# Optimization experiments

Hardware: AMD Instinct MI355X
Metric: run time of the kernel (lower is better)

Reference implementation:

```python
import jax, jax.numpy as jnp
import numpy as np

B, N, M = 2, 8192, 8192


def setup_inputs() -> dict:
    key = jax.random.key(0)
    ks = jax.random.split(key, 6)
    return {
        "predicted_points": jax.random.normal(ks[0], (B, N, 3), dtype=jnp.float32),
        "predicted_sdfs": jax.random.normal(ks[1], (B, N, 1), dtype=jnp.float32),
        "predicted_colors": jax.random.uniform(ks[2], (B, N, 3), dtype=jnp.float32),
        "ref_points": jax.random.normal(ks[3], (B, M, 3), dtype=jnp.float32),
        "ref_sdfs": jax.random.normal(ks[4], (B, M, 1), dtype=jnp.float32),
        "ref_colors": jax.random.uniform(ks[5], (B, M, 3), dtype=jnp.float32),
    }


def reference(predicted_points, predicted_sdfs, predicted_colors,
              ref_points, ref_sdfs, ref_colors):
    # Squared pairwise distances [B, N, M]; monotonic in cdist, so argmin/min
    # match torch.cdist-based results (chamfer_distance uses squared dists).
    d2 = (jnp.sum(predicted_points ** 2, axis=-1)[:, :, None]
          + jnp.sum(ref_points ** 2, axis=-1)[:, None, :]
          - 2.0 * jnp.einsum("bnd,bmd->bnm", predicted_points, ref_points))
    d2 = jnp.maximum(d2, 0.0)

    # Faithful to original: argmin over dim=1 -> nearest PREDICTED point index
    # for each ref point, shape [B, M]; then gathers into ref_sdfs/ref_colors.
    closest = jnp.argmin(d2, axis=1)  # [B, M], values in [0, N)

    gathered_sdfs = jnp.take_along_axis(ref_sdfs, closest[..., None], axis=1)  # [B, M, 1]
    sdf_l1 = jnp.mean(jnp.abs(gathered_sdfs - predicted_sdfs))

    gathered_colors = jnp.take_along_axis(ref_colors, closest[..., None], axis=1)  # [B, M, 3]
    color_l1 = jnp.mean(jnp.abs(gathered_colors - predicted_colors))

    # pytorch3d chamfer_distance: mean over points of squared min dists in both
    # directions, summed, then mean over batch.
    cham_xy = jnp.mean(jnp.min(d2, axis=2), axis=1)  # pred -> ref, [B]
    cham_yx = jnp.mean(jnp.min(d2, axis=1), axis=1)  # ref -> pred, [B]
    chamfer = jnp.mean(cham_xy + cham_yx)

    # [sdf_l1_loss, color_l1_loss, chamfer_distance_loss]
    return jnp.stack([sdf_l1, color_l1, chamfer])
```

## Files before the change

kernel.cpp:

```cpp
#include <hip/hip_runtime.h>
#include <cstdint>
#include <cstddef>

#define B_ 2
#define N_ 8192
#define M_ 8192
#define COLSPLIT 8
#define CCHUNK (N_ / COLSPLIT)
#define NTILES (CCHUNK / 32)
#define ROWS_PER_WAVE 32
#define ROWS_PER_BLOCK 128
#define RBLOCKS ((B_ * M_) / 256)

typedef __attribute__((ext_vector_type(8))) short short8;
typedef __attribute__((ext_vector_type(16))) float f32x16;

union FragU { uint4 u; short8 s; };

__device__ __forceinline__ unsigned bf16r(float f) {
    unsigned u = __float_as_uint(f);
    return ((u + 0x7FFFu + ((u >> 16) & 1u)) >> 16) & 0xFFFFu;
}
#define BF_ONE 0x3F80u

__device__ __forceinline__ unsigned umin_(unsigned a, unsigned b) { return a < b ? a : b; }

__global__ __launch_bounds__(256) void k_init(uint4* __restrict__ p)
{
    const int i = blockIdx.x * 256 + threadIdx.x;
    uint4 v = {0xFFFFFFFFu, 0xFFFFFFFFu, 0xFFFFFFFFu, 0xFFFFFFFFu};
    p[i] = v;
}

__global__ __launch_bounds__(256, 4) void k_pairs(
    const float* __restrict__ pred_pts,
    const float* __restrict__ ref_pts,
    unsigned long long* __restrict__ packed,
    unsigned int* __restrict__ colminU)
{
    __shared__ uint4 ldsB[CCHUNK + 1];
    __shared__ unsigned int ldsCol[CCHUNK];

    const int t    = threadIdx.x;
    const int wave = t >> 6;
    const int lane = t & 63;
    const int l31  = lane & 31;
    const int half = lane >> 5;
    const int rowblk  = blockIdx.x;
    const int colbase = blockIdx.y * CCHUNK;
    const int b       = blockIdx.z;

    for (int i = t; i < CCHUNK; i += 256) {
        const float* p = pred_pts + ((size_t)b * N_ + colbase + i) * 3;
        float x = p[0], y = p[1], z = p[2];
        float nrm = x * x + y * y + z * z;
        unsigned nh = bf16r(nrm);
        unsigned nl = bf16r(nrm - __uint_as_float(nh << 16));
        uint4 v;
        v.x = bf16r(-2.f * x) | (bf16r(-2.f * y) << 16);
        v.y = bf16r(-2.f * z) | (BF_ONE << 16);
        v.z = BF_ONE | (nh << 16);
        v.w = nl;
        ldsB[i] = v;
        ldsCol[i] = 0xFFFFFFFFu;
    }
    if (t == 0) { uint4 z4 = {0, 0, 0, 0}; ldsB[CCHUNK] = z4; }

    FragU af; af.u.x = af.u.y = af.u.z = af.u.w = 0;
    const int rowbase = rowblk * ROWS_PER_BLOCK + wave * ROWS_PER_WAVE;
    if (half == 0) {
        const float* r = ref_pts + ((size_t)b * M_ + rowbase + l31) * 3;
        float x = r[0], y = r[1], z = r[2];
        float nrm = x * x + y * y + z * z;
        unsigned nh = bf16r(nrm);
        unsigned nl = bf16r(nrm - __uint_as_float(nh << 16));
        af.u.x = bf16r(x) | (bf16r(y) << 16);
        af.u.y = bf16r(z) | (nh << 16);
        af.u.z = nl | (BF_ONE << 16);
        af.u.w = BF_ONE;
    }
    __syncthreads();

    f32x16 zero16 = {};
    unsigned rowbest[16];
    #pragma unroll
    for (int i = 0; i < 16; ++i) rowbest[i] = 0xFFFFFFFFu;

    const int bslot = (half == 0) ? l31 : CCHUNK;
    const int bstep = (half == 0) ? 32 : 0;

    #pragma unroll 2
    for (int tile = 0; tile < NTILES; tile += 2) {
        FragU b0; b0.u = ldsB[bslot + tile * bstep];
        FragU b1; b1.u = ldsB[bslot + (tile + 1) * bstep];
        f32x16 acc0 = __builtin_amdgcn_mfma_f32_32x32x16_bf16(af.s, b0.s, zero16, 0, 0, 0);
        f32x16 acc1 = __builtin_amdgcn_mfma_f32_32x32x16_bf16(af.s, b1.s, zero16, 0, 0, 0);

        const unsigned lcol0 = (unsigned)(tile * 32 + l31);
        const unsigned lcol1 = lcol0 + 32;
        #pragma unroll
        for (int i = 0; i < 16; ++i) {
            unsigned pk0 = (__float_as_uint(acc0[i]) & 0xFFFFF800u) | lcol0;
            unsigned pk1 = (__float_as_uint(acc1[i]) & 0xFFFFF800u) | lcol1;
            rowbest[i] = umin_(rowbest[i], umin_(pk0, pk1));
        }
        float c0 = fminf(fminf(fminf(fminf(acc0[0], acc0[1]), fminf(acc0[2], acc0[3])),
                               fminf(fminf(acc0[4], acc0[5]), fminf(acc0[6], acc0[7]))),
                         fminf(fminf(fminf(acc0[8], acc0[9]), fminf(acc0[10], acc0[11])),
                               fminf(fminf(acc0[12], acc0[13]), fminf(acc0[14], acc0[15]))));
        float c1 = fminf(fminf(fminf(fminf(acc1[0], acc1[1]), fminf(acc1[2], acc1[3])),
                               fminf(fminf(acc1[4], acc1[5]), fminf(acc1[6], acc1[7]))),
                         fminf(fminf(fminf(acc1[8], acc1[9]), fminf(acc1[10], acc1[11])),
                               fminf(fminf(acc1[12], acc1[13]), fminf(acc1[14], acc1[15]))));
        atomicMin(&ldsCol[lcol0], __float_as_uint(c0));
        atomicMin(&ldsCol[lcol1], __float_as_uint(c1));
    }

    #pragma unroll
    for (int i = 0; i < 16; ++i) {
        unsigned pk = rowbest[i];
        #pragma unroll
        for (int off = 1; off < 32; off <<= 1) {
            unsigned o = __shfl_xor(pk, off);
            pk = o < pk ? o : pk;
        }
        if (l31 == 0) {
            int row = rowbase + (i & 3) + 8 * (i >> 2) + 4 * half;
            unsigned long long v =
                ((unsigned long long)(pk & 0xFFFFF800u) << 32)
                | (unsigned)(colbase + (pk & 0x7FFu));
            atomicMin(&packed[(size_t)b * M_ + row], v);
        }
    }

    __syncthreads();
    for (int i = t; i < CCHUNK; i += 256)
        atomicMin(&colminU[(size_t)b * N_ + colbase + i], ldsCol[i]);
}

__global__ __launch_bounds__(256) void k_reduce(
    const unsigned long long* __restrict__ packed,
    const unsigned int* __restrict__ colminU,
    const float* __restrict__ pred_sdfs,
    const float* __restrict__ pred_cols,
    const float* __restrict__ ref_sdfs,
    const float* __restrict__ ref_cols,
    float* __restrict__ partials)
{
    __shared__ float wsum[4][3];
    const int i = blockIdx.x * 256 + threadIdx.x;
    const int b = i >> 13;

    unsigned long long pk = packed[i];
    float chyx = fmaxf(__uint_as_float((unsigned)(pk >> 32)), 0.f);
    int arg = (int)(unsigned)(pk & 0xFFFFFFFFull);
    float chxy = fmaxf(__uint_as_float(colminU[i]), 0.f);

    float sdf = fabsf(ref_sdfs[(size_t)b * M_ + arg] - pred_sdfs[i]);
    const float* rc = ref_cols + ((size_t)b * M_ + arg) * 3;
    const float* pc = pred_cols + (size_t)i * 3;
    float col = fabsf(rc[0] - pc[0]) + fabsf(rc[1] - pc[1]) + fabsf(rc[2] - pc[2]);

    float cham = chyx * (1.f / (B_ * M_)) + chxy * (1.f / (B_ * N_));
    sdf *= 1.f / (B_ * M_);
    col *= 1.f / (B_ * M_ * 3);

    #pragma unroll
    for (int off = 32; off > 0; off >>= 1) {
        sdf  += __shfl_down(sdf, off);
        col  += __shfl_down(col, off);
        cham += __shfl_down(cham, off);
    }
    const int wave = threadIdx.x >> 6;
    if ((threadIdx.x & 63) == 0) {
        wsum[wave][0] = sdf; wsum[wave][1] = col; wsum[wave][2] = cham;
    }
    __syncthreads();
    if (threadIdx.x == 0) {
        partials[0 * RBLOCKS + blockIdx.x] = wsum[0][0] + wsum[1][0] + wsum[2][0] + wsum[3][0];
        partials[1 * RBLOCKS + blockIdx.x] = wsum[0][1] + wsum[1][1] + wsum[2][1] + wsum[3][1];
        partials[2 * RBLOCKS + blockIdx.x] = wsum[0][2] + wsum[1][2] + wsum[2][2] + wsum[3][2];
    }
}

__global__ void k_final(const float* __restrict__ partials, float* __restrict__ out)
{
    const int t = threadIdx.x;
    float s0 = partials[0 * RBLOCKS + t];
    float s1 = partials[1 * RBLOCKS + t];
    float s2 = partials[2 * RBLOCKS + t];
    #pragma unroll
    for (int off = 32; off > 0; off >>= 1) {
        s0 += __shfl_down(s0, off);
        s1 += __shfl_down(s1, off);
        s2 += __shfl_down(s2, off);
    }
    if (t == 0) { out[0] = s0; out[1] = s1; out[2] = s2; }
}

extern "C" void kernel_launch(void* const* d_in, const int* in_sizes, int n_in,
                              void* d_out, int out_size, void* d_ws, size_t ws_size,
                              hipStream_t stream) {
    const float* pred_pts  = (const float*)d_in[0];
    const float* pred_sdfs = (const float*)d_in[1];
    const float* pred_cols = (const float*)d_in[2];
    const float* ref_pts   = (const float*)d_in[3];
    const float* ref_sdfs  = (const float*)d_in[4];
    const float* ref_cols  = (const float*)d_in[5];
    float* out = (float*)d_out;

    char* ws = (char*)d_ws;
    unsigned long long* packed = (unsigned long long*)ws;
    unsigned int* colminU = (unsigned int*)(ws + (size_t)B_ * M_ * 8);
    float* partials = (float*)(ws + (size_t)B_ * M_ * 8 + (size_t)B_ * N_ * 4);

    k_init<<<48, 256, 0, stream>>>((uint4*)ws);

    dim3 g1(M_ / ROWS_PER_BLOCK, COLSPLIT, B_);
    k_pairs<<<g1, 256, 0, stream>>>(pred_pts, ref_pts, packed, colminU);

    k_reduce<<<RBLOCKS, 256, 0, stream>>>(
        packed, colminU, pred_sdfs, pred_cols, ref_sdfs, ref_cols, partials);

    k_final<<<1, 64, 0, stream>>>(partials, out);
}
```

Before: 90.12 us.

## Replace global atomics with per-split partial buffers and drop init/final kernels

```diff
diff --git a/kernel.cpp b/kernel.cpp
--- a/kernel.cpp
+++ b/kernel.cpp
@@ -8,8 +8,7 @@
 #define COLSPLIT 8
 #define CCHUNK (N_ / COLSPLIT)
 #define NTILES (CCHUNK / 32)
-#define ROWS_PER_WAVE 32
-#define ROWS_PER_BLOCK 128
+#define ROWBLKS (M_ / 128)
 #define RBLOCKS ((B_ * M_) / 256)
 
 typedef __attribute__((ext_vector_type(8))) short short8;
@@ -24,19 +23,14 @@
 #define BF_ONE 0x3F80u
 
 __device__ __forceinline__ unsigned umin_(unsigned a, unsigned b) { return a < b ? a : b; }
-
-__global__ __launch_bounds__(256) void k_init(uint4* __restrict__ p)
-{
-    const int i = blockIdx.x * 256 + threadIdx.x;
-    uint4 v = {0xFFFFFFFFu, 0xFFFFFFFFu, 0xFFFFFFFFu, 0xFFFFFFFFu};
-    p[i] = v;
-}
+__device__ __forceinline__ unsigned long long ullmin_(unsigned long long a, unsigned long long b) { return a < b ? a : b; }
 
 __global__ __launch_bounds__(256, 4) void k_pairs(
     const float* __restrict__ pred_pts,
     const float* __restrict__ ref_pts,
-    unsigned long long* __restrict__ packed,
-    unsigned int* __restrict__ colminU)
+    unsigned long long* __restrict__ rowpart,
+    unsigned int* __restrict__ colpart,
+    float* __restrict__ out)
 {
     __shared__ uint4 ldsB[CCHUNK + 1];
     __shared__ unsigned int ldsCol[CCHUNK];
@@ -47,8 +41,13 @@
     const int l31  = lane & 31;
     const int half = lane >> 5;
     const int rowblk  = blockIdx.x;
-    const int colbase = blockIdx.y * CCHUNK;
+    const int cs      = blockIdx.y;
+    const int colbase = cs * CCHUNK;
     const int b       = blockIdx.z;
+
+    if (rowblk == 0 && cs == 0 && b == 0 && t == 0) {
+        out[0] = 0.f; out[1] = 0.f; out[2] = 0.f;
+    }
 
     for (int i = t; i < CCHUNK; i += 256) {
         const float* p = pred_pts + ((size_t)b * N_ + colbase + i) * 3;
@@ -67,7 +66,7 @@
     if (t == 0) { uint4 z4 = {0, 0, 0, 0}; ldsB[CCHUNK] = z4; }
 
     FragU af; af.u.x = af.u.y = af.u.z = af.u.w = 0;
-    const int rowbase = rowblk * ROWS_PER_BLOCK + wave * ROWS_PER_WAVE;
+    const int rowbase = rowblk * 128 + wave * 32;
     if (half == 0) {
         const float* r = ref_pts + ((size_t)b * M_ + rowbase + l31) * 3;
         float x = r[0], y = r[1], z = r[2];
@@ -116,6 +115,7 @@
         atomicMin(&ldsCol[lcol1], __float_as_uint(c1));
     }
 
+    unsigned long long* rdst = rowpart + (size_t)(b * COLSPLIT + cs) * M_;
     #pragma unroll
     for (int i = 0; i < 16; ++i) {
         unsigned pk = rowbest[i];
@@ -126,35 +126,47 @@
         }
         if (l31 == 0) {
             int row = rowbase + (i & 3) + 8 * (i >> 2) + 4 * half;
-            unsigned long long v =
-                ((unsigned long long)(pk & 0xFFFFF800u) << 32)
-                | (unsigned)(colbase + (pk & 0x7FFu));
-            atomicMin(&packed[(size_t)b * M_ + row], v);
+            rdst[row] = ((unsigned long long)(pk & 0xFFFFF800u) << 32)
+                        | (unsigned)(colbase + (pk & 0x7FFu));
         }
     }
 
     __syncthreads();
+    unsigned int* cdst = colpart + ((size_t)(b * COLSPLIT + cs) * ROWBLKS + rowblk) * CCHUNK;
     for (int i = t; i < CCHUNK; i += 256)
-        atomicMin(&colminU[(size_t)b * N_ + colbase + i], ldsCol[i]);
+        cdst[i] = ldsCol[i];
 }
 
 __global__ __launch_bounds__(256) void k_reduce(
-    const unsigned long long* __restrict__ packed,
-    const unsigned int* __restrict__ colminU,
+    const unsigned long long* __restrict__ rowpart,
+    const unsigned int* __restrict__ colpart,
     const float* __restrict__ pred_sdfs,
     const float* __restrict__ pred_cols,
     const float* __restrict__ ref_sdfs,
     const float* __restrict__ ref_cols,
-    float* __restrict__ partials)
+    float* __restrict__ out)
 {
     __shared__ float wsum[4][3];
     const int i = blockIdx.x * 256 + threadIdx.x;
     const int b = i >> 13;
-
-    unsigned long long pk = packed[i];
+    const int m = i & (M_ - 1);
+
+    unsigned long long pk = 0xFFFFFFFFFFFFFFFFull;
+    #pragma unroll
+    for (int s = 0; s < COLSPLIT; ++s)
+        pk = ullmin_(pk, rowpart[(size_t)(b * COLSPLIT + s) * M_ + m]);
+
+    const int cs = m >> 10;
+    const int c  = m & (CCHUNK - 1);
+    const unsigned int* cp = colpart + (size_t)(b * COLSPLIT + cs) * ROWBLKS * CCHUNK + c;
+    unsigned cm = 0xFFFFFFFFu;
+    #pragma unroll 8
+    for (int rb = 0; rb < ROWBLKS; ++rb)
+        cm = umin_(cm, cp[(size_t)rb * CCHUNK]);
+
     float chyx = fmaxf(__uint_as_float((unsigned)(pk >> 32)), 0.f);
     int arg = (int)(unsigned)(pk & 0xFFFFFFFFull);
-    float chxy = fmaxf(__uint_as_float(colminU[i]), 0.f);
+    float chxy = fmaxf(__uint_as_float(cm), 0.f);
 
     float sdf = fabsf(ref_sdfs[(size_t)b * M_ + arg] - pred_sdfs[i]);
     const float* rc = ref_cols + ((size_t)b * M_ + arg) * 3;
@@ -177,25 +189,10 @@
     }
     __syncthreads();
     if (threadIdx.x == 0) {
-        partials[0 * RBLOCKS + blockIdx.x] = wsum[0][0] + wsum[1][0] + wsum[2][0] + wsum[3][0];
-        partials[1 * RBLOCKS + blockIdx.x] = wsum[0][1] + wsum[1][1] + wsum[2][1] + wsum[3][1];
-        partials[2 * RBLOCKS + blockIdx.x] = wsum[0][2] + wsum[1][2] + wsum[2][2] + wsum[3][2];
-    }
-}
-
-__global__ void k_final(const float* __restrict__ partials, float* __restrict__ out)
-{
-    const int t = threadIdx.x;
-    float s0 = partials[0 * RBLOCKS + t];
-    float s1 = partials[1 * RBLOCKS + t];
-    float s2 = partials[2 * RBLOCKS + t];
-    #pragma unroll
-    for (int off = 32; off > 0; off >>= 1) {
-        s0 += __shfl_down(s0, off);
-        s1 += __shfl_down(s1, off);
-        s2 += __shfl_down(s2, off);
-    }
-    if (t == 0) { out[0] = s0; out[1] = s1; out[2] = s2; }
+        atomicAdd(&out[0], wsum[0][0] + wsum[1][0] + wsum[2][0] + wsum[3][0]);
+        atomicAdd(&out[1], wsum[0][1] + wsum[1][1] + wsum[2][1] + wsum[3][1]);
+        atomicAdd(&out[2], wsum[0][2] + wsum[1][2] + wsum[2][2] + wsum[3][2]);
+    }
 }
 
 extern "C" void kernel_launch(void* const* d_in, const int* in_sizes, int n_in,
@@ -210,17 +207,12 @@
     float* out = (float*)d_out;
 
     char* ws = (char*)d_ws;
-    unsigned long long* packed = (unsigned long long*)ws;
-    unsigned int* colminU = (unsigned int*)(ws + (size_t)B_ * M_ * 8);
-    float* partials = (float*)(ws + (size_t)B_ * M_ * 8 + (size_t)B_ * N_ * 4);
-
-    k_init<<<48, 256, 0, stream>>>((uint4*)ws);
-
-    dim3 g1(M_ / ROWS_PER_BLOCK, COLSPLIT, B_);
-    k_pairs<<<g1, 256, 0, stream>>>(pred_pts, ref_pts, packed, colminU);
+    unsigned long long* rowpart = (unsigned long long*)ws;
+    unsigned int* colpart = (unsigned int*)(ws + (size_t)B_ * COLSPLIT * M_ * 8);
+
+    dim3 g1(ROWBLKS, COLSPLIT, B_);
+    k_pairs<<<g1, 256, 0, stream>>>(pred_pts, ref_pts, rowpart, colpart, out);
 
     k_reduce<<<RBLOCKS, 256, 0, stream>>>(
-        packed, colminU, pred_sdfs, pred_cols, ref_sdfs, ref_cols, partials);
-
-    k_final<<<1, 64, 0, stream>>>(partials, out);
-}
+        rowpart, colpart, pred_sdfs, pred_cols, ref_sdfs, ref_cols, out);
+}
```

Measured after the change: 93.12 us. 1.03x slower.
